# Kernel optimization log

Measured on AMD Instinct MI355X. Metric: run time of the kernel, lower is better.

The kernel has to match this reference:

```python
import math
import jax, jax.numpy as jnp
import numpy as np

B, S, H = 4, 4096, 1024
NH, HD = 16, 64
MLP_DIM = 4096


def _gelu_tanh(x):
    c = math.sqrt(2.0 / math.pi)
    return 0.5 * x * (1.0 + jnp.tanh(c * (x + 0.044715 * x * x * x)))


def _layernorm(x, w, b, eps=1e-5):
    mu = jnp.mean(x, axis=-1, keepdims=True)
    var = jnp.var(x, axis=-1, keepdims=True)
    return (x - mu) * jax.lax.rsqrt(var + eps) * w + b


def setup_inputs() -> dict:
    key = jax.random.key(0)
    ks = jax.random.split(key, 12)
    s = 0.02
    return {
        "x": jax.random.normal(ks[0], (B, S, H), jnp.float32),
        "ln1_w": jnp.ones((H,), jnp.float32),
        "ln1_b": jnp.zeros((H,), jnp.float32),
        "q_w": jax.random.normal(ks[1], (H, H), jnp.float32) * s,
        "q_b": jnp.zeros((H,), jnp.float32),
        "k_w": jax.random.normal(ks[2], (H, H), jnp.float32) * s,
        "k_b": jnp.zeros((H,), jnp.float32),
        "v_w": jax.random.normal(ks[3], (H, H), jnp.float32) * s,
        "v_b": jnp.zeros((H,), jnp.float32),
        "o_w": jax.random.normal(ks[4], (H, H), jnp.float32) * s,
        "o_b": jnp.zeros((H,), jnp.float32),
        "ln2_w": jnp.ones((H,), jnp.float32),
        "ln2_b": jnp.zeros((H,), jnp.float32),
        "fc_w": jax.random.normal(ks[5], (H, MLP_DIM), jnp.float32) * s,
        "fc_b": jnp.zeros((MLP_DIM,), jnp.float32),
        "proj_w": jax.random.normal(ks[6], (MLP_DIM, H), jnp.float32) * (s / math.sqrt(2 * 12)),
        "proj_b": jnp.zeros((H,), jnp.float32),
    }


def reference(x, ln1_w, ln1_b, q_w, q_b, k_w, k_b, v_w, v_b, o_w, o_b,
              ln2_w, ln2_b, fc_w, fc_b, proj_w, proj_b):
    bsz, seqlen, h = x.shape
    ln_x = _layernorm(x, ln1_w, ln1_b)

    # projections -> [b, nh, t, hd]
    def heads(y):
        return y.reshape(bsz, seqlen, NH, HD).transpose(0, 2, 1, 3)

    q = heads(ln_x @ q_w + q_b)
    k = heads(ln_x @ k_w + k_b)
    v = heads(ln_x @ v_w + v_b)

    # feature map: elu(x)+1
    qf = jax.nn.elu(q) + 1.0
    kf = jax.nn.elu(k) + 1.0

    kv = jnp.einsum('bhtd,bhte->bhde', kf, v)              # [b,nh,hd,hd]
    norm = 1.0 / (jnp.einsum('bhtd,bhd->bht', qf, kf.sum(axis=2)) + 1e-6)
    out = jnp.einsum('bhtd,bhde->bhte', qf, kv) * norm[..., None]
    out = out.transpose(0, 2, 1, 3).reshape(bsz, seqlen, h)
    attn = out @ o_w + o_b

    x = x + attn
    h_mlp = _gelu_tanh(_layernorm(x, ln2_w, ln2_b) @ fc_w + fc_b)
    x = x + (h_mlp @ proj_w + proj_b)
    return x
```

## Files before the change

### kernel.cpp

```cpp
#include <hip/hip_runtime.h>
#include <hip/hip_bf16.h>
#include <cstdint>
#include <cstddef>

typedef __bf16 bf16;
typedef __bf16 bf16x8 __attribute__((ext_vector_type(8)));
typedef __bf16 bf16x4 __attribute__((ext_vector_type(4)));
typedef float  f32x4  __attribute__((ext_vector_type(4)));

typedef __attribute__((address_space(1))) void gvoid_t;
typedef __attribute__((address_space(3))) void lvoid_t;

#define GLD_LDS16(g, l) __builtin_amdgcn_global_load_lds( \
    (gvoid_t*)(uintptr_t)(g), (lvoid_t*)(uint32_t)(uintptr_t)(l), 16, 0, 0)

#define SBAR() __builtin_amdgcn_s_barrier()
#define WAIT_VM0() asm volatile("s_waitcnt vmcnt(0)" ::: "memory")

__global__ __launch_bounds__(256) void transpose_cast(
    const float* __restrict__ in, bf16* __restrict__ out, int R, int C)
{
  __shared__ float tile[32][33];
  const int bx = blockIdx.x;
  const int by = blockIdx.y;
  const int tx = threadIdx.x;
  const int ty = threadIdx.y;
#pragma unroll
  for (int i = 0; i < 32; i += 8)
    tile[ty + i][tx] = in[(size_t)(by * 32 + ty + i) * C + bx * 32 + tx];
  __syncthreads();
#pragma unroll
  for (int i = 0; i < 32; i += 8)
    out[(size_t)(bx * 32 + ty + i) * R + by * 32 + tx] = (bf16)tile[tx][ty + i];
}

__global__ __launch_bounds__(256) void ln_row(
    const float* __restrict__ x, const float* __restrict__ w,
    const float* __restrict__ b, bf16* __restrict__ out)
{
  const int row = blockIdx.x;
  const int tid = threadIdx.x;
  const float4 v = ((const float4*)(x + (size_t)row * 1024))[tid];
  float s  = v.x + v.y + v.z + v.w;
  float ss = v.x * v.x + v.y * v.y + v.z * v.z + v.w * v.w;
#pragma unroll
  for (int off = 32; off > 0; off >>= 1) {
    s  += __shfl_down(s, off);
    ss += __shfl_down(ss, off);
  }
  __shared__ float red[8];
  const int wid = tid >> 6, lane = tid & 63;
  if (lane == 0) { red[wid] = s; red[4 + wid] = ss; }
  __syncthreads();
  s  = red[0] + red[1] + red[2] + red[3];
  ss = red[4] + red[5] + red[6] + red[7];
  const float mu   = s * (1.f / 1024.f);
  const float var  = ss * (1.f / 1024.f) - mu * mu;
  const float rstd = rsqrtf(var + 1e-5f);
  const float4 wv = ((const float4*)w)[tid];
  const float4 bv = ((const float4*)b)[tid];
  bf16x4 ov;
  ov[0] = (bf16)((v.x - mu) * rstd * wv.x + bv.x);
  ov[1] = (bf16)((v.y - mu) * rstd * wv.y + bv.y);
  ov[2] = (bf16)((v.z - mu) * rstd * wv.z + bv.z);
  ov[3] = (bf16)((v.w - mu) * rstd * wv.w + bv.w);
  *(bf16x4*)(out + (size_t)row * 1024 + tid * 4) = ov;
}

template <int EPI>
__global__ __launch_bounds__(512, 2) void gemm256(
    const bf16* __restrict__ A, const bf16* __restrict__ BT,
    const float* __restrict__ bias, const float* __restrict__ resid,
    void* __restrict__ outp, int M, int N, int K, int nx)
{
  __shared__ __align__(16) char lds[131072];
  const int tid  = threadIdx.x;
  const int wid  = tid >> 6, lane = tid & 63;
  const int wr   = wid >> 2, wc = wid & 3;
  const int ln15 = lane & 15, lhi = lane >> 4;

  const int nwg = (int)gridDim.x;
  const int cpx = nwg >> 3;
  const int bid = (int)blockIdx.x;
  const int lg  = (bid & 7) * cpx + (bid >> 3);
  const int bx  = lg % nx, by = lg / nx;
  const int row0 = by << 8, col0 = bx << 8;

  const int srow  = tid >> 3;
  const int sslot = (tid & 7) ^ (srow & 7);
  const bf16* aS = A  + (size_t)(row0 + srow) * K + sslot * 8;
  const bf16* bS = BT + (size_t)(col0 + srow) * K + sslot * 8;
  const size_t rjump = (size_t)K << 6;
  char* ldsW = lds + wid * 1024;

  const int rAb = (wr << 7) + ln15;
  const int rBb = (wc << 6) + ln15;
  const int sl0 = lhi ^ (ln15 & 7);
  const int sl1 = (4 + lhi) ^ (ln15 & 7);
  const int aOff0 = rAb * 128 + sl0 * 16;
  const int aOff1 = rAb * 128 + sl1 * 16;
  const int bOff0 = rBb * 128 + sl0 * 16 + 65536;
  const int bOff1 = rBb * 128 + sl1 * 16 + 65536;

  f32x4 acc[8][4] = {};
  const int nt = K >> 6;

#define STG(D, KT) do { \
    const bf16* ga_ = aS + (size_t)(KT) * 64; \
    const bf16* gb_ = bS + (size_t)(KT) * 64; \
    char* la_ = ldsW + (D) * 32768; \
    char* lb_ = la_ + 65536; \
    GLD_LDS16(ga_,             la_);         GLD_LDS16(gb_,             lb_); \
    GLD_LDS16(ga_ + rjump,     la_ + 8192);  GLD_LDS16(gb_ + rjump,     lb_ + 8192); \
    GLD_LDS16(ga_ + 2 * rjump, la_ + 16384); GLD_LDS16(gb_ + 2 * rjump, lb_ + 16384); \
    GLD_LDS16(ga_ + 3 * rjump, la_ + 24576); GLD_LDS16(gb_ + 3 * rjump, lb_ + 24576); \
  } while (0)

  STG(0, 0);
  WAIT_VM0();
  SBAR();

  for (int kt = 0; kt < nt; ++kt) {
    const int d = kt & 1;
    const char* base = (const char*)lds + d * 32768;
    if (kt + 1 < nt) STG(d ^ 1, kt + 1);

    bf16x8 a0[8], b0[4], a1[8], b1[4];
#pragma unroll
    for (int m = 0; m < 8; ++m) a0[m] = *(const bf16x8*)(base + aOff0 + m * 2048);
#pragma unroll
    for (int n = 0; n < 4; ++n) b0[n] = *(const bf16x8*)(base + bOff0 + n * 2048);
#pragma unroll
    for (int m = 0; m < 8; ++m) a1[m] = *(const bf16x8*)(base + aOff1 + m * 2048);
#pragma unroll
    for (int n = 0; n < 4; ++n) b1[n] = *(const bf16x8*)(base + bOff1 + n * 2048);

    __builtin_amdgcn_s_setprio(1);
#pragma unroll
    for (int m = 0; m < 8; ++m)
#pragma unroll
      for (int n = 0; n < 4; ++n)
        acc[m][n] = __builtin_amdgcn_mfma_f32_16x16x32_bf16(a0[m], b0[n], acc[m][n], 0, 0, 0);
#pragma unroll
    for (int m = 0; m < 8; ++m)
#pragma unroll
      for (int n = 0; n < 4; ++n)
        acc[m][n] = __builtin_amdgcn_mfma_f32_16x16x32_bf16(a1[m], b1[n], acc[m][n], 0, 0, 0);
    __builtin_amdgcn_s_setprio(0);

    WAIT_VM0();
    SBAR();
  }
#undef STG

  const int lr4 = lhi << 2;
#pragma unroll
  for (int m = 0; m < 8; ++m) {
#pragma unroll
    for (int n = 0; n < 4; ++n) {
      const int c_i = col0 + wc * 64 + n * 16 + ln15;
      const float bv = bias[c_i];
#pragma unroll
      for (int j = 0; j < 4; ++j) {
        const int r_i = row0 + wr * 128 + m * 16 + lr4 + j;
        const size_t idx = (size_t)r_i * N + c_i;
        float val = acc[m][n][j] + bv;
        if constexpr (EPI == 0) {
          ((bf16*)outp)[idx] = (bf16)val;
        } else if constexpr (EPI == 1) {
          ((bf16*)outp)[idx] = (bf16)(val > 0.f ? val + 1.f : __expf(val));
        } else if constexpr (EPI == 2) {
          ((float*)outp)[idx] = val + resid[idx];
        } else {
          const float u  = 0.7978845608028654f * (val + 0.044715f * val * val * val);
          const float th = 1.f - 2.f / (__expf(2.f * u) + 1.f);
          ((bf16*)outp)[idx] = (bf16)(0.5f * val * (1.f + th));
        }
      }
    }
  }
}

__global__ __launch_bounds__(256) void kv_part_kernel(
    const bf16* __restrict__ kf, const bf16* __restrict__ v,
    float* __restrict__ kv_part, float* __restrict__ ksum_part)
{
  const int bh = blockIdx.x >> 3, ch = blockIdx.x & 7;
  const int b = bh >> 4, h = bh & 15;
  const int tid = threadIdx.x;
  const int e = tid & 63, dg = tid >> 6;
  const size_t grow0 = (size_t)b * 4096 + (size_t)ch * 512;
  const size_t cbase = (size_t)h * 64;
  __shared__ bf16 skf[8][64], sv[8][64];
  float accum[16];
#pragma unroll
  for (int i = 0; i < 16; ++i) accum[i] = 0.f;
  float ks = 0.f;
  const int tt = tid >> 5, cc = (tid & 31) << 1;
  for (int t0 = 0; t0 < 512; t0 += 8) {
    __syncthreads();
    const size_t base = (grow0 + t0 + tt) * 1024 + cbase + cc;
    *(uint32_t*)&skf[tt][cc] = *(const uint32_t*)(kf + base);
    *(uint32_t*)&sv[tt][cc]  = *(const uint32_t*)(v + base);
    __syncthreads();
#pragma unroll
    for (int q = 0; q < 8; ++q) {
      const float vv = (float)sv[q][e];
#pragma unroll
      for (int dd = 0; dd < 16; ++dd)
        accum[dd] += (float)skf[q][dg * 16 + dd] * vv;
    }
    if (tid < 64) {
#pragma unroll
      for (int q = 0; q < 8; ++q) ks += (float)skf[q][tid];
    }
  }
  float* op = kv_part + (size_t)blockIdx.x * 4096 + (size_t)(dg * 16) * 64 + e;
#pragma unroll
  for (int dd = 0; dd < 16; ++dd) op[dd * 64] = accum[dd];
  if (tid < 64) ksum_part[(size_t)blockIdx.x * 64 + tid] = ks;
}

__global__ __launch_bounds__(256) void kv_reduce(
    const float* __restrict__ kvp, const float* __restrict__ ksp,
    float* __restrict__ kvf, float* __restrict__ ksf)
{
  const int bh = blockIdx.x;
  const int tid = threadIdx.x;
  for (int i = tid; i < 4096; i += 256) {
    float s = 0.f;
#pragma unroll
    for (int ch = 0; ch < 8; ++ch) s += kvp[((size_t)bh * 8 + ch) * 4096 + i];
    kvf[(size_t)bh * 4096 + i] = s;
  }
  if (tid < 64) {
    float s = 0.f;
#pragma unroll
    for (int ch = 0; ch < 8; ++ch) s += ksp[((size_t)bh * 8 + ch) * 64 + tid];
    ksf[(size_t)bh * 64 + tid] = s;
  }
}

__global__ __launch_bounds__(256) void attn_out_kernel(
    const bf16* __restrict__ qf, const float* __restrict__ kvf,
    const float* __restrict__ ksf, bf16* __restrict__ attn)
{
  const int bh = blockIdx.x >> 6, rb = blockIdx.x & 63;
  const int b = bh >> 4, h = bh & 15;
  const int tid = threadIdx.x;
  const int e = tid & 63, rbase = (tid >> 6) << 4;
  __shared__ __align__(16) bf16 sqf[64][64];
  __shared__ float sks[64];
  const size_t grow0 = (size_t)b * 4096 + (size_t)rb * 64;

  {
    const int rr = tid >> 2, c0 = (tid & 3) << 4;
    const bf16* src = qf + (grow0 + rr) * 1024 + h * 64 + c0;
    *(bf16x8*)&sqf[rr][c0]     = *(const bf16x8*)src;
    *(bf16x8*)&sqf[rr][c0 + 8] = *(const bf16x8*)(src + 8);
  }
  if (tid < 64) sks[tid] = ksf[(size_t)bh * 64 + tid];

  float kcol[64];
#pragma unroll
  for (int d = 0; d < 64; ++d) kcol[d] = kvf[(size_t)bh * 4096 + d * 64 + e];

  __syncthreads();

  for (int rr = 0; rr < 16; ++rr) {
    const int r = rbase + rr;
    bf16x8 q8[8];
#pragma unroll
    for (int i = 0; i < 8; ++i) q8[i] = *(const bf16x8*)&sqf[r][i * 8];
    float sk = 0.f, sv = 0.f;
#pragma unroll
    for (int i = 0; i < 8; ++i)
#pragma unroll
      for (int jj = 0; jj < 8; ++jj) {
        const float qd = (float)q8[i][jj];
        sk += qd * sks[i * 8 + jj];
        sv += qd * kcol[i * 8 + jj];
      }
    attn[(grow0 + r) * 1024 + h * 64 + e] = (bf16)(sv / (sk + 1e-6f));
  }
}

extern "C" void kernel_launch(void* const* d_in, const int* in_sizes, int n_in,
                              void* d_out, int out_size, void* d_ws, size_t ws_size,
                              hipStream_t stream)
{
  const float* x    = (const float*)d_in[0];
  const float* ln1w = (const float*)d_in[1];
  const float* ln1b = (const float*)d_in[2];
  const float* qw   = (const float*)d_in[3];
  const float* qb   = (const float*)d_in[4];
  const float* kw   = (const float*)d_in[5];
  const float* kb   = (const float*)d_in[6];
  const float* vw   = (const float*)d_in[7];
  const float* vb   = (const float*)d_in[8];
  const float* ow   = (const float*)d_in[9];
  const float* ob   = (const float*)d_in[10];
  const float* ln2w = (const float*)d_in[11];
  const float* ln2b = (const float*)d_in[12];
  const float* fcw  = (const float*)d_in[13];
  const float* fcb  = (const float*)d_in[14];
  const float* pjw  = (const float*)d_in[15];
  const float* pjb  = (const float*)d_in[16];
  float* out = (float*)d_out;
  char* ws = (char*)d_ws;

  constexpr size_t O_LNX  = 0;
  constexpr size_t O_QF   = 33554432;
  constexpr size_t O_KF   = 67108864;
  constexpr size_t O_V    = 100663296;
  constexpr size_t O_HMLP = 0;
  constexpr size_t O_KVP  = 134217728;
  constexpr size_t O_KSP  = 142606336;
  constexpr size_t O_KVF  = 142737408;
  constexpr size_t O_KSF  = 143785984;
  constexpr size_t O_ATTN = 143802368;
  constexpr size_t O_LN2  = 177356800;
  constexpr size_t O_WQ   = 210911232;
  constexpr size_t O_WK   = 213008384;
  constexpr size_t O_WV   = 215105536;
  constexpr size_t O_WO   = 217202688;
  constexpr size_t O_WFC  = 219299840;
  constexpr size_t O_WPJ  = 227688448;

  bf16* lnx  = (bf16*)(ws + O_LNX);
  bf16* qfb  = (bf16*)(ws + O_QF);
  bf16* kfb  = (bf16*)(ws + O_KF);
  bf16* vbuf = (bf16*)(ws + O_V);
  bf16* hmlp = (bf16*)(ws + O_HMLP);
  float* kvp = (float*)(ws + O_KVP);
  float* ksp = (float*)(ws + O_KSP);
  float* kvf = (float*)(ws + O_KVF);
  float* ksf = (float*)(ws + O_KSF);
  bf16* attn = (bf16*)(ws + O_ATTN);
  bf16* ln2h = (bf16*)(ws + O_LN2);
  bf16* wqT  = (bf16*)(ws + O_WQ);
  bf16* wkT  = (bf16*)(ws + O_WK);
  bf16* wvT  = (bf16*)(ws + O_WV);
  bf16* woT  = (bf16*)(ws + O_WO);
  bf16* wfcT = (bf16*)(ws + O_WFC);
  bf16* wpjT = (bf16*)(ws + O_WPJ);

  const dim3 tb(32, 8);
  transpose_cast<<<dim3(32, 32),  tb, 0, stream>>>(qw,  wqT, 1024, 1024);
  transpose_cast<<<dim3(32, 32),  tb, 0, stream>>>(kw,  wkT, 1024, 1024);
  transpose_cast<<<dim3(32, 32),  tb, 0, stream>>>(vw,  wvT, 1024, 1024);
  transpose_cast<<<dim3(32, 32),  tb, 0, stream>>>(ow,  woT, 1024, 1024);
  transpose_cast<<<dim3(128, 32), tb, 0, stream>>>(fcw, wfcT, 1024, 4096);
  transpose_cast<<<dim3(32, 128), tb, 0, stream>>>(pjw, wpjT, 4096, 1024);

  ln_row<<<16384, 256, 0, stream>>>(x, ln1w, ln1b, lnx);

  gemm256<1><<<256, 512, 0, stream>>>(lnx, wqT, qb, nullptr, qfb, 16384, 1024, 1024, 4);
  gemm256<1><<<256, 512, 0, stream>>>(lnx, wkT, kb, nullptr, kfb, 16384, 1024, 1024, 4);
  gemm256<0><<<256, 512, 0, stream>>>(lnx, wvT, vb, nullptr, vbuf, 16384, 1024, 1024, 4);

  kv_part_kernel<<<512, 256, 0, stream>>>(kfb, vbuf, kvp, ksp);
  kv_reduce<<<64, 256, 0, stream>>>(kvp, ksp, kvf, ksf);
  attn_out_kernel<<<4096, 256, 0, stream>>>(qfb, kvf, ksf, attn);

  gemm256<2><<<256, 512, 0, stream>>>(attn, woT, ob, x, out, 16384, 1024, 1024, 4);

  ln_row<<<16384, 256, 0, stream>>>(out, ln2w, ln2b, ln2h);

  gemm256<3><<<1024, 512, 0, stream>>>(ln2h, wfcT, fcb, nullptr, hmlp, 16384, 4096, 1024, 16);

  gemm256<2><<<256, 512, 0, stream>>>(hmlp, wpjT, pjb, out, out, 16384, 1024, 4096, 4);
}
```

Before: 720.6 us.

## Fuse QKV projections into one GEMM and deepen GEMM prefetch pipeline

Concatenates the transposed Q, K and V weights and their biases so a single 16384x3072 GEMM produces an interleaved QKV buffer, with a new epilogue that applies elu+1 only to the Q and K columns. The kv and attention-output kernels now read from the strided QKV buffer. Separately, the GEMM main loop now prefetches two K-tiles ahead: it issues the next stage after the LDS reads and a barrier, and uses a partial vmcnt wait instead of draining all loads. The fused GEMM reads the LN output once instead of three times and launches one wider grid. The stride-3072 reads in the attention kernels and the extra barrier per iteration could cost some of that back.

```diff
diff --git a/kernel.cpp b/kernel.cpp
--- a/kernel.cpp
+++ b/kernel.cpp
@@ -15,7 +15,10 @@
     (gvoid_t*)(uintptr_t)(g), (lvoid_t*)(uint32_t)(uintptr_t)(l), 16, 0, 0)
 
 #define SBAR() __builtin_amdgcn_s_barrier()
+#define SCHED_FENCE() __builtin_amdgcn_sched_barrier(0)
 #define WAIT_VM0() asm volatile("s_waitcnt vmcnt(0)" ::: "memory")
+#define WAIT_VM8() asm volatile("s_waitcnt vmcnt(8)" ::: "memory")
+#define WAIT_LGKM0() asm volatile("s_waitcnt lgkmcnt(0)" ::: "memory")
 
 __global__ __launch_bounds__(256) void transpose_cast(
     const float* __restrict__ in, bf16* __restrict__ out, int R, int C)
@@ -32,6 +35,14 @@
 #pragma unroll
   for (int i = 0; i < 32; i += 8)
     out[(size_t)(bx * 32 + ty + i) * R + by * 32 + tx] = (bf16)tile[tx][ty + i];
+}
+
+__global__ __launch_bounds__(256) void pack3(
+    const float* __restrict__ a, const float* __restrict__ b,
+    const float* __restrict__ c, float* __restrict__ o)
+{
+  const int i = blockIdx.x * 256 + threadIdx.x;
+  o[i] = i < 1024 ? a[i] : (i < 2048 ? b[i - 1024] : c[i - 2048]);
 }
 
 __global__ __launch_bounds__(256) void ln_row(
@@ -117,13 +128,13 @@
   } while (0)
 
   STG(0, 0);
-  WAIT_VM0();
+  STG(1, 1);
+  WAIT_VM8();
   SBAR();
 
   for (int kt = 0; kt < nt; ++kt) {
     const int d = kt & 1;
     const char* base = (const char*)lds + d * 32768;
-    if (kt + 1 < nt) STG(d ^ 1, kt + 1);
 
     bf16x8 a0[8], b0[4], a1[8], b1[4];
 #pragma unroll
@@ -134,6 +145,11 @@
     for (int m = 0; m < 8; ++m) a1[m] = *(const bf16x8*)(base + aOff1 + m * 2048);
 #pragma unroll
     for (int n = 0; n < 4; ++n) b1[n] = *(const bf16x8*)(base + bOff1 + n * 2048);
+
+    WAIT_LGKM0();
+    SBAR();
+    if (kt + 2 < nt) STG(d, kt + 2);
+    SCHED_FENCE();
 
     __builtin_amdgcn_s_setprio(1);
 #pragma unroll
@@ -148,7 +164,8 @@
         acc[m][n] = __builtin_amdgcn_mfma_f32_16x16x32_bf16(a1[m], b1[n], acc[m][n], 0, 0, 0);
     __builtin_amdgcn_s_setprio(0);
 
-    WAIT_VM0();
+    if (kt + 2 < nt) { WAIT_VM8(); }
+    else if (kt + 1 < nt) { WAIT_VM0(); }
     SBAR();
   }
 #undef STG
@@ -171,10 +188,15 @@
           ((bf16*)outp)[idx] = (bf16)(val > 0.f ? val + 1.f : __expf(val));
         } else if constexpr (EPI == 2) {
           ((float*)outp)[idx] = val + resid[idx];
-        } else {
+        } else if constexpr (EPI == 3) {
           const float u  = 0.7978845608028654f * (val + 0.044715f * val * val * val);
           const float th = 1.f - 2.f / (__expf(2.f * u) + 1.f);
           ((bf16*)outp)[idx] = (bf16)(0.5f * val * (1.f + th));
+        } else {
+          if (c_i < 2048)
+            ((bf16*)outp)[idx] = (bf16)(val > 0.f ? val + 1.f : __expf(val));
+          else
+            ((bf16*)outp)[idx] = (bf16)val;
         }
       }
     }
@@ -182,15 +204,15 @@
 }
 
 __global__ __launch_bounds__(256) void kv_part_kernel(
-    const bf16* __restrict__ kf, const bf16* __restrict__ v,
-    float* __restrict__ kv_part, float* __restrict__ ksum_part)
+    const bf16* __restrict__ qkv, float* __restrict__ kv_part,
+    float* __restrict__ ksum_part)
 {
   const int bh = blockIdx.x >> 3, ch = blockIdx.x & 7;
   const int b = bh >> 4, h = bh & 15;
   const int tid = threadIdx.x;
   const int e = tid & 63, dg = tid >> 6;
   const size_t grow0 = (size_t)b * 4096 + (size_t)ch * 512;
-  const size_t cbase = (size_t)h * 64;
+  const size_t kbase = 1024 + (size_t)h * 64;
   __shared__ bf16 skf[8][64], sv[8][64];
   float accum[16];
 #pragma unroll
@@ -199,9 +221,9 @@
   const int tt = tid >> 5, cc = (tid & 31) << 1;
   for (int t0 = 0; t0 < 512; t0 += 8) {
     __syncthreads();
-    const size_t base = (grow0 + t0 + tt) * 1024 + cbase + cc;
-    *(uint32_t*)&skf[tt][cc] = *(const uint32_t*)(kf + base);
-    *(uint32_t*)&sv[tt][cc]  = *(const uint32_t*)(v + base);
+    const size_t base = (grow0 + t0 + tt) * 3072 + kbase + cc;
+    *(uint32_t*)&skf[tt][cc] = *(const uint32_t*)(qkv + base);
+    *(uint32_t*)&sv[tt][cc]  = *(const uint32_t*)(qkv + base + 1024);
     __syncthreads();
 #pragma unroll
     for (int q = 0; q < 8; ++q) {
@@ -242,7 +264,7 @@
 }
 
 __global__ __launch_bounds__(256) void attn_out_kernel(
-    const bf16* __restrict__ qf, const float* __restrict__ kvf,
+    const bf16* __restrict__ qkv, const float* __restrict__ kvf,
     const float* __restrict__ ksf, bf16* __restrict__ attn)
 {
   const int bh = blockIdx.x >> 6, rb = blockIdx.x & 63;
@@ -255,7 +277,7 @@
 
   {
     const int rr = tid >> 2, c0 = (tid & 3) << 4;
-    const bf16* src = qf + (grow0 + rr) * 1024 + h * 64 + c0;
+    const bf16* src = qkv + (grow0 + rr) * 3072 + h * 64 + c0;
     *(bf16x8*)&sqf[rr][c0]     = *(const bf16x8*)src;
     *(bf16x8*)&sqf[rr][c0 + 8] = *(const bf16x8*)(src + 8);
   }
@@ -310,9 +332,7 @@
   char* ws = (char*)d_ws;
 
   constexpr size_t O_LNX  = 0;
-  constexpr size_t O_QF   = 33554432;
-  constexpr size_t O_KF   = 67108864;
-  constexpr size_t O_V    = 100663296;
+  constexpr size_t O_QKV  = 33554432;
   constexpr size_t O_HMLP = 0;
   constexpr size_t O_KVP  = 134217728;
   constexpr size_t O_KSP  = 142606336;
@@ -321,47 +341,41 @@
   constexpr size_t O_ATTN = 143802368;
   constexpr size_t O_LN2  = 177356800;
   constexpr size_t O_WQ   = 210911232;
-  constexpr size_t O_WK   = 213008384;
-  constexpr size_t O_WV   = 215105536;
   constexpr size_t O_WO   = 217202688;
   constexpr size_t O_WFC  = 219299840;
   constexpr size_t O_WPJ  = 227688448;
 
-  bf16* lnx  = (bf16*)(ws + O_LNX);
-  bf16* qfb  = (bf16*)(ws + O_QF);
-  bf16* kfb  = (bf16*)(ws + O_KF);
-  bf16* vbuf = (bf16*)(ws + O_V);
-  bf16* hmlp = (bf16*)(ws + O_HMLP);
-  float* kvp = (float*)(ws + O_KVP);
-  float* ksp = (float*)(ws + O_KSP);
-  float* kvf = (float*)(ws + O_KVF);
-  float* ksf = (float*)(ws + O_KSF);
-  bf16* attn = (bf16*)(ws + O_ATTN);
-  bf16* ln2h = (bf16*)(ws + O_LN2);
-  bf16* wqT  = (bf16*)(ws + O_WQ);
-  bf16* wkT  = (bf16*)(ws + O_WK);
-  bf16* wvT  = (bf16*)(ws + O_WV);
-  bf16* woT  = (bf16*)(ws + O_WO);
-  bf16* wfcT = (bf16*)(ws + O_WFC);
-  bf16* wpjT = (bf16*)(ws + O_WPJ);
+  bf16* lnx   = (bf16*)(ws + O_LNX);
+  bf16* qkv   = (bf16*)(ws + O_QKV);
+  bf16* hmlp  = (bf16*)(ws + O_HMLP);
+  float* kvp  = (float*)(ws + O_KVP);
+  float* qkvb = (float*)(ws + O_KVP);
+  float* ksp  = (float*)(ws + O_KSP);
+  float* kvf  = (float*)(ws + O_KVF);
+  float* ksf  = (float*)(ws + O_KSF);
+  bf16* attn  = (bf16*)(ws + O_ATTN);
+  bf16* ln2h  = (bf16*)(ws + O_LN2);
+  bf16* wqkvT = (bf16*)(ws + O_WQ);
+  bf16* woT   = (bf16*)(ws + O_WO);
+  bf16* wfcT  = (bf16*)(ws + O_WFC);
+  bf16* wpjT  = (bf16*)(ws + O_WPJ);
 
   const dim3 tb(32, 8);
-  transpose_cast<<<dim3(32, 32),  tb, 0, stream>>>(qw,  wqT, 1024, 1024);
-  transpose_cast<<<dim3(32, 32),  tb, 0, stream>>>(kw,  wkT, 1024, 1024);
-  transpose_cast<<<dim3(32, 32),  tb, 0, stream>>>(vw,  wvT, 1024, 1024);
+  transpose_cast<<<dim3(32, 32),  tb, 0, stream>>>(qw,  wqkvT,                1024, 1024);
+  transpose_cast<<<dim3(32, 32),  tb, 0, stream>>>(kw,  wqkvT + 1024 * 1024,  1024, 1024);
+  transpose_cast<<<dim3(32, 32),  tb, 0, stream>>>(vw,  wqkvT + 2048 * 1024,  1024, 1024);
   transpose_cast<<<dim3(32, 32),  tb, 0, stream>>>(ow,  woT, 1024, 1024);
   transpose_cast<<<dim3(128, 32), tb, 0, stream>>>(fcw, wfcT, 1024, 4096);
   transpose_cast<<<dim3(32, 128), tb, 0, stream>>>(pjw, wpjT, 4096, 1024);
+  pack3<<<12, 256, 0, stream>>>(qb, kb, vb, qkvb);
 
   ln_row<<<16384, 256, 0, stream>>>(x, ln1w, ln1b, lnx);
 
-  gemm256<1><<<256, 512, 0, stream>>>(lnx, wqT, qb, nullptr, qfb, 16384, 1024, 1024, 4);
-  gemm256<1><<<256, 512, 0, stream>>>(lnx, wkT, kb, nullptr, kfb, 16384, 1024, 1024, 4);
-  gemm256<0><<<256, 512, 0, stream>>>(lnx, wvT, vb, nullptr, vbuf, 16384, 1024, 1024, 4);
-
-  kv_part_kernel<<<512, 256, 0, stream>>>(kfb, vbuf, kvp, ksp);
+  gemm256<4><<<768, 512, 0, stream>>>(lnx, wqkvT, qkvb, nullptr, qkv, 16384, 3072, 1024, 12);
+
+  kv_part_kernel<<<512, 256, 0, stream>>>(qkv, kvp, ksp);
   kv_reduce<<<64, 256, 0, stream>>>(kvp, ksp, kvf, ksf);
-  attn_out_kernel<<<4096, 256, 0, stream>>>(qfb, kvf, ksf, attn);
+  attn_out_kernel<<<4096, 256, 0, stream>>>(qkv, kvf, ksf, attn);
 
   gemm256<2><<<256, 512, 0, stream>>>(attn, woT, ob, x, out, 16384, 1024, 1024, 4);
 
```

Result: no change. 715.2 us (-0.8%).
